# Optimization experiments

Measured on AMD Instinct MI355X. Metric: run time of the kernel, lower is better.

## Reference

```python
import jax, jax.numpy as jnp
import numpy as np

# Dimensions: batch B, window W (time features), nodes M, hidden HID, hops NLAYERS
B, W, M, HID, NLAYERS = 32, 168, 2048, 128, 6


def setup_inputs() -> dict:
    key = jax.random.key(0)
    ks = jax.random.split(key, 6)
    x = jax.random.normal(ks[0], (B, W, M), dtype=jnp.float32)
    # scale L so matrix powers L^k stay bounded (spectral radius < 1)
    L = jax.random.normal(ks[1], (M, M), dtype=jnp.float32) / (2.0 * np.float32(np.sqrt(M)))
    # stacked per-hop MLP params: linears[i]: W->HID, linears2[i]: HID->1
    W1 = jax.random.normal(ks[2], (NLAYERS + 1, HID, W), dtype=jnp.float32) / np.float32(np.sqrt(W))
    b1 = jax.random.normal(ks[3], (NLAYERS + 1, HID), dtype=jnp.float32) * 0.01
    W2 = jax.random.normal(ks[4], (NLAYERS + 1, HID), dtype=jnp.float32) / np.float32(np.sqrt(HID))
    b2 = jax.random.normal(ks[5], (NLAYERS + 1,), dtype=jnp.float32) * 0.01
    return {"x": x, "L": L, "W1": W1, "b1": b1, "W2": W2, "b2": b2}


def _hop_mlp(t, w1, bb1, w2, bb2):
    # t: [B, M, W] -> scalar score per node: Linear(W->HID), ReLU, Linear(HID->1)
    h = jax.nn.relu(jnp.einsum('bmw,hw->bmh', t, w1) + bb1)
    return jnp.einsum('bmh,h->bm', h, w2) + bb2


def reference(x, L, W1, b1, W2, b2):
    xt = jnp.swapaxes(x, 1, 2)  # [B, M, W] (x.transpose(2,1))
    s = _hop_mlp(xt, W1[0], b1[0], W2[0], b2[0])  # [B, M]
    P = L
    for i in range(1, NLAYERS + 1):
        # PP.expand + bmm == broadcasted matmul; never materialize [B,M,M]
        t = jnp.einsum('ij,bjw->biw', P, xt)  # [B, M, W]
        s = s + _hop_mlp(t, W1[i], b1[i], W2[i], b2[i])
        P = jnp.matmul(L, P)  # next graph power
    return s  # [B, M]; output_fun is None so no final nonlinearity
```

## Files before the change

### kernel.cpp

```cpp
#include <hip/hip_runtime.h>
#include <cstdint>
#include <cstddef>

typedef __bf16 bf16_t;
typedef __attribute__((ext_vector_type(8))) __bf16 bf16x8;
typedef __attribute__((ext_vector_type(4))) __bf16 bf16x4;
typedef __attribute__((ext_vector_type(4))) float floatx4;

#define NB 32
#define NW 168
#define NM 2048
#define NHID 128
#define NBW (NB * NW)
#define NGEMM 168
#define NMLPB 512

#define GLOAD_LDS16(g, l)                                          \
  __builtin_amdgcn_global_load_lds(                                \
      (const __attribute__((address_space(1))) void*)(g),          \
      (__attribute__((address_space(3))) void*)(l), 16, 0, 0)

__global__ void cast_bf16_kernel(const float* __restrict__ in, bf16_t* __restrict__ out, int n4) {
  int stride = gridDim.x * blockDim.x;
  for (int i = blockIdx.x * blockDim.x + threadIdx.x; i < n4; i += stride) {
    float4 v = ((const float4*)in)[i];
    bf16x4 o = {(bf16_t)v.x, (bf16_t)v.y, (bf16_t)v.z, (bf16_t)v.w};
    ((bf16x4*)out)[i] = o;
  }
}

__global__ void prep_x_kernel(const float* __restrict__ x, bf16_t* __restrict__ Xb,
                              bf16_t* __restrict__ XT) {
  __shared__ float tile[64][65];
  const int R = NBW, C = NM;
  int r0 = blockIdx.y * 64, c0 = blockIdx.x * 64;
  int t = threadIdx.x;
  int tr = t >> 4, tc4 = (t & 15) * 4;
#pragma unroll
  for (int p = 0; p < 4; ++p) {
    int row = p * 16 + tr;
    float4 v = *(const float4*)(x + (size_t)(r0 + row) * C + c0 + tc4);
    tile[row][tc4 + 0] = v.x;
    tile[row][tc4 + 1] = v.y;
    tile[row][tc4 + 2] = v.z;
    tile[row][tc4 + 3] = v.w;
    bf16x4 o = {(bf16_t)v.x, (bf16_t)v.y, (bf16_t)v.z, (bf16_t)v.w};
    *(bf16x4*)(Xb + (size_t)(r0 + row) * C + c0 + tc4) = o;
  }
  __syncthreads();
#pragma unroll
  for (int p = 0; p < 4; ++p) {
    int c = p * 16 + tr;
    bf16x4 o = {(bf16_t)tile[tc4 + 0][c], (bf16_t)tile[tc4 + 1][c],
                (bf16_t)tile[tc4 + 2][c], (bf16_t)tile[tc4 + 3][c]};
    *(bf16x4*)(XT + (size_t)(c0 + c) * R + r0 + tc4) = o;
  }
}

__device__ __forceinline__ void mlp_single(
    int tid, int r0, bf16_t* __restrict__ Bs,
    const bf16_t* __restrict__ T, const bf16_t* __restrict__ Wh,
    const float* __restrict__ b1h, const float* __restrict__ w2h, float b2v,
    float* __restrict__ out, int accumulate) {
  float* sred = (float*)(Bs + 24576);
  int lane = tid & 63, wv2 = tid >> 6;

#pragma unroll
  for (int i = 0; i < 6; ++i) {
    int c = i * 512 + tid;
    if (c >= 2688) {
      int4 z = {0, 0, 0, 0};
      *(int4*)(Bs + (size_t)c * 8) = z;
    } else {
      int kc = c >> 7;
      int h = (c & 127) ^ ((kc & 3) << 2);
      GLOAD_LDS16(Wh + (size_t)h * NW + kc * 8, Bs + (size_t)(i * 512 + wv2 * 64) * 8);
    }
  }
  __syncthreads();

  if (tid < 256) {
    int wm = wv2 >> 1, wn = wv2 & 1;
    int quad = lane >> 4, l15 = lane & 15;
    const bf16_t* arow[4];
#pragma unroll
    for (int mi = 0; mi < 4; ++mi) {
      int R = r0 + wm * 64 + mi * 16 + l15;
      arow[mi] = T + (size_t)(R >> 5) * NBW + (size_t)(R & 31) * NW + quad * 8;
    }
    floatx4 zero4 = {0.f, 0.f, 0.f, 0.f};
    floatx4 acc[4][4];
#pragma unroll
    for (int mi = 0; mi < 4; ++mi)
#pragma unroll
      for (int ni = 0; ni < 4; ++ni) acc[mi][ni] = zero4;

#pragma unroll
    for (int kb = 0; kb < 192; kb += 32) {
      int kc = (kb >> 3) + quad;
      bf16x8 af[4], bf[4];
#pragma unroll
      for (int mi = 0; mi < 4; ++mi)
        af[mi] = *(const bf16x8*)(arow[mi] + kb);
#pragma unroll
      for (int ni = 0; ni < 4; ++ni) {
        int hpos = (wn * 64 + ni * 16 + l15) ^ ((kc & 3) << 2);
        bf[ni] = *(const bf16x8*)(Bs + (size_t)(kc * 128 + hpos) * 8);
      }
#pragma unroll
      for (int mi = 0; mi < 4; ++mi)
#pragma unroll
        for (int ni = 0; ni < 4; ++ni)
          acc[mi][ni] = __builtin_amdgcn_mfma_f32_16x16x32_bf16(af[mi], bf[ni], acc[mi][ni], 0, 0, 0);
    }

    float part[4][4];
#pragma unroll
    for (int mi = 0; mi < 4; ++mi)
#pragma unroll
      for (int r = 0; r < 4; ++r) part[mi][r] = 0.f;
#pragma unroll
    for (int ni = 0; ni < 4; ++ni) {
      int col = wn * 64 + ni * 16 + l15;
      float b1v = b1h[col];
      float w2v = w2h[col];
#pragma unroll
      for (int mi = 0; mi < 4; ++mi)
#pragma unroll
        for (int r = 0; r < 4; ++r) {
          float h = acc[mi][ni][r] + b1v;
          h = h > 0.f ? h : 0.f;
          part[mi][r] += h * w2v;
        }
    }
#pragma unroll
    for (int off = 1; off < 16; off <<= 1)
#pragma unroll
      for (int mi = 0; mi < 4; ++mi)
#pragma unroll
        for (int r = 0; r < 4; ++r) part[mi][r] += __shfl_xor(part[mi][r], off);
    if (l15 == 0) {
#pragma unroll
      for (int mi = 0; mi < 4; ++mi)
#pragma unroll
        for (int r = 0; r < 4; ++r) sred[wv2 * 64 + mi * 16 + quad * 4 + r] = part[mi][r];
    }
  }
  __syncthreads();
  if (tid < 128) {
    int hh = tid >> 6;
    int lr = tid & 63;
    float v = sred[(hh * 2) * 64 + lr] + sred[(hh * 2 + 1) * 64 + lr] + b2v;
    int R = r0 + hh * 64 + lr;
    int idx = (R & 31) * NM + (R >> 5);
    if (accumulate)
      out[idx] += v;
    else
      out[idx] = v;
  }
}

#define STAGE2(gbase, ld, t, ks, ldsbase)                                        \
  do {                                                                           \
    const bf16_t* _g = (gbase) + (size_t)(t) * 64 + (ks) * 32;                   \
    GLOAD_LDS16(_g, lds + (ldsbase) + (ks) * 8192 + wv * 512);                   \
    GLOAD_LDS16(_g + (size_t)128 * (ld),                                         \
                lds + (ldsbase) + (ks) * 8192 + 4096 + wv * 512);                \
  } while (0)

#define VM6 asm volatile("s_waitcnt vmcnt(6)" ::: "memory")
#define TOPB asm volatile("s_barrier" ::: "memory")
#define ENDB __builtin_amdgcn_s_barrier()

#define RD_A(dst, bufoff, ks, mh)                                                \
  _Pragma("unroll") for (int mi = 0; mi < 4; ++mi)                               \
      dst[mi] = *(const bf16x8*)(pA + (bufoff) + (ks) * 8192 + ((mh) * 4 + mi) * 512)

#define RD_B(dst, bufoff, ks)                                                    \
  _Pragma("unroll") for (int ni = 0; ni < 4; ++ni)                               \
      dst[ni] = *(const bf16x8*)(pB + (bufoff) + (ks) * 8192 + ni * 512)

#define MM16(af_, bf_, mh)                                                       \
  do {                                                                           \
    __builtin_amdgcn_s_setprio(1);                                               \
    _Pragma("unroll") for (int mi = 0; mi < 4; ++mi)                             \
        _Pragma("unroll") for (int ni = 0; ni < 4; ++ni)                         \
            acc[(mh) * 4 + mi][ni] = __builtin_amdgcn_mfma_f32_16x16x32_bf16(    \
                af_[mi], bf_[ni], acc[(mh) * 4 + mi][ni], 0, 0, 0);              \
    __builtin_amdgcn_s_setprio(0);                                               \
  } while (0)

__global__ __launch_bounds__(512, 2) void fused_gemm_mlp_kernel(
    const bf16_t* __restrict__ A, const bf16_t* __restrict__ Bt,
    bf16_t* __restrict__ C, bf16_t* __restrict__ Ct,
    int K, int lda, int ldb, int ldc, int ldct, int write_c,
    const bf16_t* __restrict__ T, const bf16_t* __restrict__ W1b,
    const float* __restrict__ b1, const float* __restrict__ W2,
    const float* __restrict__ b2, float* __restrict__ out,
    int hop, int accumulate) {
  __shared__ bf16_t lds[65536];
  const int bx = blockIdx.x;
  const int tid = threadIdx.x;

  if (bx >= NGEMM) {
    int j = bx - NGEMM;
    mlp_single(tid, j * 128, lds, T, W1b + (size_t)hop * NHID * NW,
               b1 + hop * NHID, W2 + hop * NHID, b2[hop], out, accumulate);
    return;
  }

  const int m0 = (bx >> 3) * 256, n0 = (bx & 7) * 256;
  const int lane = tid & 63, wv = tid >> 6;
  const int wm = wv >> 2, wn = wv & 3;
  const int quad = lane >> 4, l15 = lane & 15;

  const int srow = tid >> 2;
  const int scsw = (tid & 3) ^ ((srow >> 1) & 3);
  const bf16_t* aS = A + (size_t)(m0 + srow) * lda + scsw * 8;
  const bf16_t* bS = Bt + (size_t)(n0 + srow) * ldb + scsw * 8;

  const int fsw = (quad ^ ((l15 >> 1) & 3)) * 8;
  const bf16_t* pA = lds + (size_t)(wm * 128 + l15) * 32 + fsw;
  const bf16_t* pB = lds + 16384 + (size_t)(wn * 64 + l15) * 32 + fsw;

  floatx4 zero4 = {0.f, 0.f, 0.f, 0.f};
  floatx4 acc[8][4];
#pragma unroll
  for (int mi = 0; mi < 8; ++mi)
#pragma unroll
    for (int ni = 0; ni < 4; ++ni) acc[mi][ni] = zero4;

  STAGE2(aS, lda, 0, 0, 0);
  STAGE2(bS, ldb, 0, 0, 16384);
  STAGE2(aS, lda, 0, 1, 0);
  STAGE2(bS, ldb, 0, 1, 16384);
  STAGE2(aS, lda, 1, 0, 32768);
  STAGE2(bS, ldb, 1, 0, 49152);
  asm volatile("s_waitcnt vmcnt(8)" ::: "memory");
  TOPB;

  bf16x8 af0[4], af1[4], bf0[4], bf1[4];
  RD_B(bf0, 0, 0);
  RD_A(af0, 0, 0, 0);

  const int nt = K >> 6;
  const int nit = K >> 7;
#pragma unroll 1
  for (int i = 0; i < nit; ++i) {
    const int t1 = 2 * i + 1;
    const int t2 = (t1 + 1 < nt) ? t1 + 1 : 0;
    const int t3 = (t1 + 2 < nt) ? t1 + 2 : 0;
    RD_A(af1, 0, 0, 1);
    MM16(af0, bf0, 0);
    STAGE2(aS, lda, t1, 1, 32768);
    ENDB;
    VM6; TOPB;
    RD_B(bf1, 0, 1);
    RD_A(af0, 0, 1, 0);
    MM16(af1, bf0, 1);
    STAGE2(bS, ldb, t1, 1, 49152);
    ENDB;
    RD_A(af1, 0, 1, 1);
    MM16(af0, bf1, 0);
    STAGE2(aS, lda, t2, 0, 0);
    ENDB;
    VM6; TOPB;
    RD_B(bf0, 32768, 0);
    RD_A(af0, 32768, 0, 0);
    MM16(af1, bf1, 1);
    STAGE2(bS, ldb, t2, 0, 16384);
    ENDB;
    RD_A(af1, 32768, 0, 1);
    MM16(af0, bf0, 0);
    STAGE2(aS, lda, t2, 1, 0);
    ENDB;
    VM6; TOPB;
    RD_B(bf1, 32768, 1);
    RD_A(af0, 32768, 1, 0);
    MM16(af1, bf0, 1);
    STAGE2(bS, ldb, t2, 1, 16384);
    ENDB;
    RD_A(af1, 32768, 1, 1);
    MM16(af0, bf1, 0);
    STAGE2(aS, lda, t3, 0, 32768);
    ENDB;
    VM6; TOPB;
    RD_B(bf0, 0, 0);
    RD_A(af0, 0, 0, 0);
    MM16(af1, bf1, 1);
    STAGE2(bS, ldb, t3, 0, 49152);
    ENDB;
  }
  asm volatile("s_waitcnt vmcnt(0)" ::: "memory");

#pragma unroll
  for (int mi = 0; mi < 8; ++mi) {
#pragma unroll
    for (int ni = 0; ni < 4; ++ni) {
      int col = n0 + wn * 64 + ni * 16 + l15;
      int rowb = m0 + wm * 128 + mi * 16 + quad * 4;
      bf16x4 tv;
#pragma unroll
      for (int r = 0; r < 4; ++r) tv[r] = (bf16_t)acc[mi][ni][r];
      *(bf16x4*)(Ct + (size_t)col * ldct + rowb) = tv;
      if (write_c) {
#pragma unroll
        for (int r = 0; r < 4; ++r)
          C[(size_t)(rowb + r) * ldc + col] = tv[r];
      }
    }
  }
}

__global__ __launch_bounds__(512) void mlp_score_kernel(
    const bf16_t* __restrict__ T, const bf16_t* __restrict__ W1b,
    const float* __restrict__ b1, const float* __restrict__ W2,
    const float* __restrict__ b2, float* __restrict__ out,
    int hop, int accumulate) {
  __shared__ bf16_t Bs[24 * 128 * 8 + 512];
  mlp_single(threadIdx.x, blockIdx.x * 128, Bs, T,
             W1b + (size_t)hop * NHID * NW, b1 + hop * NHID, W2 + hop * NHID,
             b2[hop], out, accumulate);
}

extern "C" void kernel_launch(void* const* d_in, const int* in_sizes, int n_in,
                              void* d_out, int out_size, void* d_ws, size_t ws_size,
                              hipStream_t stream) {
  const float* x = (const float*)d_in[0];
  const float* L = (const float*)d_in[1];
  const float* W1 = (const float*)d_in[2];
  const float* b1 = (const float*)d_in[3];
  const float* W2 = (const float*)d_in[4];
  const float* b2 = (const float*)d_in[5];
  float* out = (float*)d_out;

  char* ws = (char*)d_ws;
  size_t off = 0;
  auto walloc = [&](size_t bytes) -> void* {
    off = (off + 255) & ~(size_t)255;
    void* p = ws + off;
    off += bytes;
    return p;
  };
  bf16_t* Xb = (bf16_t*)walloc((size_t)NBW * NM * 2);
  bf16_t* XT0 = (bf16_t*)walloc((size_t)NM * NBW * 2);
  bf16_t* XT1 = (bf16_t*)walloc((size_t)NM * NBW * 2);
  bf16_t* Lb = (bf16_t*)walloc((size_t)NM * NM * 2);
  bf16_t* W1b = (bf16_t*)walloc((size_t)7 * NHID * NW * 2);
  bf16_t* Ta = (bf16_t*)walloc((size_t)NBW * NM * 2);
  (void)ws_size; (void)in_sizes; (void)n_in; (void)out_size;

  prep_x_kernel<<<dim3(NM / 64, NBW / 64), dim3(256), 0, stream>>>(x, Xb, XT0);
  cast_bf16_kernel<<<dim3(1024), dim3(256), 0, stream>>>(L, Lb, NM * NM / 4);
  cast_bf16_kernel<<<dim3(64), dim3(256), 0, stream>>>(W1, W1b, 7 * NHID * NW / 4);

  bf16_t* src = Xb;
  bf16_t* dst = Ta;
  bf16_t* xtprev = XT0;
  bf16_t* xtcur = XT1;
  for (int i = 1; i <= 6; ++i) {
    fused_gemm_mlp_kernel<<<dim3(NGEMM + NMLPB), dim3(512), 0, stream>>>(
        src, Lb, dst, xtcur, NM, NM, NM, NM, NBW, (i < 6) ? 1 : 0,
        xtprev, W1b, b1, W2, b2, out, i - 1, (i > 1) ? 1 : 0);
    bf16_t* t = src; src = dst; dst = t;
    t = xtprev; xtprev = xtcur; xtcur = t;
  }
  mlp_score_kernel<<<dim3(NM * NB / 128), dim3(512), 0, stream>>>(
      xtprev, W1b, b1, W2, b2, out, 6, 1);
}
```

Before: 466.0 us.

## Use 32x32x16 MFMA in GEMM, widen MLP blocks, merge prep kernels

Switches the main GEMM inner loop from 16x16x32 to 32x32x16 bf16 MFMA tiles, changing LDS fragment reads, swizzle and epilogue layout to match. The MLP-score path now uses all 8 waves to process 256 rows per block, which halves the number of MLP blocks. The three prep kernels (x transpose/cast, L cast, W1 cast) are merged into one launch. The aim is fewer LDS reads per FLOP, better MFMA efficiency and less launch overhead. The risks are register pressure from the floatx16 accumulators and a possible layout mismatch in the new fragment indexing.

```diff
diff --git a/kernel.cpp b/kernel.cpp
--- a/kernel.cpp
+++ b/kernel.cpp
@@ -6,6 +6,7 @@
 typedef __attribute__((ext_vector_type(8))) __bf16 bf16x8;
 typedef __attribute__((ext_vector_type(4))) __bf16 bf16x4;
 typedef __attribute__((ext_vector_type(4))) float floatx4;
+typedef __attribute__((ext_vector_type(16))) float floatx16;
 
 #define NB 32
 #define NW 168
@@ -13,51 +14,61 @@
 #define NHID 128
 #define NBW (NB * NW)
 #define NGEMM 168
-#define NMLPB 512
+#define NMLPB 256
 
 #define GLOAD_LDS16(g, l)                                          \
   __builtin_amdgcn_global_load_lds(                                \
       (const __attribute__((address_space(1))) void*)(g),          \
       (__attribute__((address_space(3))) void*)(l), 16, 0, 0)
 
-__global__ void cast_bf16_kernel(const float* __restrict__ in, bf16_t* __restrict__ out, int n4) {
-  int stride = gridDim.x * blockDim.x;
-  for (int i = blockIdx.x * blockDim.x + threadIdx.x; i < n4; i += stride) {
-    float4 v = ((const float4*)in)[i];
-    bf16x4 o = {(bf16_t)v.x, (bf16_t)v.y, (bf16_t)v.z, (bf16_t)v.w};
-    ((bf16x4*)out)[i] = o;
-  }
-}
-
-__global__ void prep_x_kernel(const float* __restrict__ x, bf16_t* __restrict__ Xb,
-                              bf16_t* __restrict__ XT) {
+__global__ void prep_all_kernel(const float* __restrict__ x, bf16_t* __restrict__ Xb,
+                                bf16_t* __restrict__ XT, const float* __restrict__ L,
+                                bf16_t* __restrict__ Lb, const float* __restrict__ W1,
+                                bf16_t* __restrict__ W1b) {
   __shared__ float tile[64][65];
-  const int R = NBW, C = NM;
-  int r0 = blockIdx.y * 64, c0 = blockIdx.x * 64;
-  int t = threadIdx.x;
-  int tr = t >> 4, tc4 = (t & 15) * 4;
-#pragma unroll
-  for (int p = 0; p < 4; ++p) {
-    int row = p * 16 + tr;
-    float4 v = *(const float4*)(x + (size_t)(r0 + row) * C + c0 + tc4);
-    tile[row][tc4 + 0] = v.x;
-    tile[row][tc4 + 1] = v.y;
-    tile[row][tc4 + 2] = v.z;
-    tile[row][tc4 + 3] = v.w;
-    bf16x4 o = {(bf16_t)v.x, (bf16_t)v.y, (bf16_t)v.z, (bf16_t)v.w};
-    *(bf16x4*)(Xb + (size_t)(r0 + row) * C + c0 + tc4) = o;
-  }
-  __syncthreads();
-#pragma unroll
-  for (int p = 0; p < 4; ++p) {
-    int c = p * 16 + tr;
-    bf16x4 o = {(bf16_t)tile[tc4 + 0][c], (bf16_t)tile[tc4 + 1][c],
-                (bf16_t)tile[tc4 + 2][c], (bf16_t)tile[tc4 + 3][c]};
-    *(bf16x4*)(XT + (size_t)(c0 + c) * R + r0 + tc4) = o;
-  }
-}
-
-__device__ __forceinline__ void mlp_single(
+  const int bx = blockIdx.x;
+  const int t = threadIdx.x;
+  if (bx < 2688) {
+    const int R = NBW, C = NM;
+    int r0 = (bx >> 5) * 64, c0 = (bx & 31) * 64;
+    int tr = t >> 4, tc4 = (t & 15) * 4;
+#pragma unroll
+    for (int p = 0; p < 4; ++p) {
+      int row = p * 16 + tr;
+      float4 v = *(const float4*)(x + (size_t)(r0 + row) * C + c0 + tc4);
+      tile[row][tc4 + 0] = v.x;
+      tile[row][tc4 + 1] = v.y;
+      tile[row][tc4 + 2] = v.z;
+      tile[row][tc4 + 3] = v.w;
+      bf16x4 o = {(bf16_t)v.x, (bf16_t)v.y, (bf16_t)v.z, (bf16_t)v.w};
+      *(bf16x4*)(Xb + (size_t)(r0 + row) * C + c0 + tc4) = o;
+    }
+    __syncthreads();
+#pragma unroll
+    for (int p = 0; p < 4; ++p) {
+      int c = p * 16 + tr;
+      bf16x4 o = {(bf16_t)tile[tc4 + 0][c], (bf16_t)tile[tc4 + 1][c],
+                  (bf16_t)tile[tc4 + 2][c], (bf16_t)tile[tc4 + 3][c]};
+      *(bf16x4*)(XT + (size_t)(c0 + c) * R + r0 + tc4) = o;
+    }
+  } else if (bx < 3712) {
+    const int n4 = NM * NM / 4;
+    for (int i = (bx - 2688) * 256 + t; i < n4; i += 1024 * 256) {
+      float4 v = ((const float4*)L)[i];
+      bf16x4 o = {(bf16_t)v.x, (bf16_t)v.y, (bf16_t)v.z, (bf16_t)v.w};
+      ((bf16x4*)Lb)[i] = o;
+    }
+  } else {
+    const int n4 = 7 * NHID * NW / 4;
+    for (int i = (bx - 3712) * 256 + t; i < n4; i += 64 * 256) {
+      float4 v = ((const float4*)W1)[i];
+      bf16x4 o = {(bf16_t)v.x, (bf16_t)v.y, (bf16_t)v.z, (bf16_t)v.w};
+      ((bf16x4*)W1b)[i] = o;
+    }
+  }
+}
+
+__device__ __forceinline__ void mlp_block(
     int tid, int r0, bf16_t* __restrict__ Bs,
     const bf16_t* __restrict__ T, const bf16_t* __restrict__ Wh,
     const float* __restrict__ b1h, const float* __restrict__ w2h, float b2v,
@@ -79,7 +90,7 @@
   }
   __syncthreads();
 
-  if (tid < 256) {
+  {
     int wm = wv2 >> 1, wn = wv2 & 1;
     int quad = lane >> 4, l15 = lane & 15;
     const bf16_t* arow[4];
@@ -147,11 +158,11 @@
     }
   }
   __syncthreads();
-  if (tid < 128) {
-    int hh = tid >> 6;
+  if (tid < 256) {
+    int wm = tid >> 6;
     int lr = tid & 63;
-    float v = sred[(hh * 2) * 64 + lr] + sred[(hh * 2 + 1) * 64 + lr] + b2v;
-    int R = r0 + hh * 64 + lr;
+    float v = sred[(wm * 2) * 64 + lr] + sred[(wm * 2 + 1) * 64 + lr] + b2v;
+    int R = r0 + wm * 64 + lr;
     int idx = (R & 31) * NM + (R >> 5);
     if (accumulate)
       out[idx] += v;
@@ -172,21 +183,27 @@
 #define TOPB asm volatile("s_barrier" ::: "memory")
 #define ENDB __builtin_amdgcn_s_barrier()
 
-#define RD_A(dst, bufoff, ks, mh)                                                \
-  _Pragma("unroll") for (int mi = 0; mi < 4; ++mi)                               \
-      dst[mi] = *(const bf16x8*)(pA + (bufoff) + (ks) * 8192 + ((mh) * 4 + mi) * 512)
-
-#define RD_B(dst, bufoff, ks)                                                    \
-  _Pragma("unroll") for (int ni = 0; ni < 4; ++ni)                               \
-      dst[ni] = *(const bf16x8*)(pB + (bufoff) + (ks) * 8192 + ni * 512)
-
-#define MM16(af_, bf_, mh)                                                       \
+#define RD_A4(dst, bufoff, ks, mh)                                               \
+  _Pragma("unroll") for (int kk = 0; kk < 2; ++kk)                               \
+      _Pragma("unroll") for (int mf = 0; mf < 2; ++mf)                           \
+          dst[kk * 2 + mf] = *(const bf16x8*)(pA + (bufoff) + (ks) * 8192 +      \
+              ((mh) * 2 + mf) * 1024 + (((kk * 2 + hi) ^ fsw32) << 3))
+
+#define RD_B4(dst, bufoff, ks)                                                   \
+  _Pragma("unroll") for (int kk = 0; kk < 2; ++kk)                               \
+      _Pragma("unroll") for (int nf = 0; nf < 2; ++nf)                           \
+          dst[kk * 2 + nf] = *(const bf16x8*)(pB + (bufoff) + (ks) * 8192 +      \
+              nf * 1024 + (((kk * 2 + hi) ^ fsw32) << 3))
+
+#define MM(af_, bf_, mh)                                                         \
   do {                                                                           \
     __builtin_amdgcn_s_setprio(1);                                               \
-    _Pragma("unroll") for (int mi = 0; mi < 4; ++mi)                             \
-        _Pragma("unroll") for (int ni = 0; ni < 4; ++ni)                         \
-            acc[(mh) * 4 + mi][ni] = __builtin_amdgcn_mfma_f32_16x16x32_bf16(    \
-                af_[mi], bf_[ni], acc[(mh) * 4 + mi][ni], 0, 0, 0);              \
+    _Pragma("unroll") for (int mf = 0; mf < 2; ++mf)                             \
+        _Pragma("unroll") for (int nf = 0; nf < 2; ++nf)                         \
+            _Pragma("unroll") for (int kk = 0; kk < 2; ++kk)                     \
+                acc[(mh) * 2 + mf][nf] = __builtin_amdgcn_mfma_f32_32x32x16_bf16(\
+                    af_[kk * 2 + mf], bf_[kk * 2 + nf], acc[(mh) * 2 + mf][nf],  \
+                    0, 0, 0);                                                    \
     __builtin_amdgcn_s_setprio(0);                                               \
   } while (0)
 
@@ -204,31 +221,32 @@
 
   if (bx >= NGEMM) {
     int j = bx - NGEMM;
-    mlp_single(tid, j * 128, lds, T, W1b + (size_t)hop * NHID * NW,
-               b1 + hop * NHID, W2 + hop * NHID, b2[hop], out, accumulate);
+    mlp_block(tid, j * 256, lds, T, W1b + (size_t)hop * NHID * NW,
+              b1 + hop * NHID, W2 + hop * NHID, b2[hop], out, accumulate);
     return;
   }
 
   const int m0 = (bx >> 3) * 256, n0 = (bx & 7) * 256;
   const int lane = tid & 63, wv = tid >> 6;
   const int wm = wv >> 2, wn = wv & 3;
-  const int quad = lane >> 4, l15 = lane & 15;
+  const int l31 = lane & 31, hi = lane >> 5;
+  const int fsw32 = (l31 >> 1) & 3;
 
   const int srow = tid >> 2;
   const int scsw = (tid & 3) ^ ((srow >> 1) & 3);
   const bf16_t* aS = A + (size_t)(m0 + srow) * lda + scsw * 8;
   const bf16_t* bS = Bt + (size_t)(n0 + srow) * ldb + scsw * 8;
 
-  const int fsw = (quad ^ ((l15 >> 1) & 3)) * 8;
-  const bf16_t* pA = lds + (size_t)(wm * 128 + l15) * 32 + fsw;
-  const bf16_t* pB = lds + 16384 + (size_t)(wn * 64 + l15) * 32 + fsw;
-
-  floatx4 zero4 = {0.f, 0.f, 0.f, 0.f};
-  floatx4 acc[8][4];
-#pragma unroll
-  for (int mi = 0; mi < 8; ++mi)
-#pragma unroll
-    for (int ni = 0; ni < 4; ++ni) acc[mi][ni] = zero4;
+  const bf16_t* pA = lds + (size_t)(wm * 128 + l31) * 32;
+  const bf16_t* pB = lds + 16384 + (size_t)(wn * 64 + l31) * 32;
+
+  floatx16 acc[4][2];
+#pragma unroll
+  for (int mf = 0; mf < 4; ++mf)
+#pragma unroll
+    for (int nf = 0; nf < 2; ++nf)
+#pragma unroll
+      for (int r = 0; r < 16; ++r) acc[mf][nf][r] = 0.f;
 
   STAGE2(aS, lda, 0, 0, 0);
   STAGE2(bS, ldb, 0, 0, 16384);
@@ -240,8 +258,8 @@
   TOPB;
 
   bf16x8 af0[4], af1[4], bf0[4], bf1[4];
-  RD_B(bf0, 0, 0);
-  RD_A(af0, 0, 0, 0);
+  RD_B4(bf0, 0, 0);
+  RD_A4(af0, 0, 0, 0);
 
   const int nt = K >> 6;
   const int nit = K >> 7;
@@ -250,63 +268,66 @@
     const int t1 = 2 * i + 1;
     const int t2 = (t1 + 1 < nt) ? t1 + 1 : 0;
     const int t3 = (t1 + 2 < nt) ? t1 + 2 : 0;
-    RD_A(af1, 0, 0, 1);
-    MM16(af0, bf0, 0);
+    RD_A4(af1, 0, 0, 1);
+    MM(af0, bf0, 0);
     STAGE2(aS, lda, t1, 1, 32768);
     ENDB;
     VM6; TOPB;
-    RD_B(bf1, 0, 1);
-    RD_A(af0, 0, 1, 0);
-    MM16(af1, bf0, 1);
+    RD_B4(bf1, 0, 1);
+    RD_A4(af0, 0, 1, 0);
+    MM(af1, bf0, 1);
     STAGE2(bS, ldb, t1, 1, 49152);
     ENDB;
-    RD_A(af1, 0, 1, 1);
-    MM16(af0, bf1, 0);
+    RD_A4(af1, 0, 1, 1);
+    MM(af0, bf1, 0);
     STAGE2(aS, lda, t2, 0, 0);
     ENDB;
     VM6; TOPB;
-    RD_B(bf0, 32768, 0);
-    RD_A(af0, 32768, 0, 0);
-    MM16(af1, bf1, 1);
+    RD_B4(bf0, 32768, 0);
+    RD_A4(af0, 32768, 0, 0);
+    MM(af1, bf1, 1);
     STAGE2(bS, ldb, t2, 0, 16384);
     ENDB;
-    RD_A(af1, 32768, 0, 1);
-    MM16(af0, bf0, 0);
+    RD_A4(af1, 32768, 0, 1);
+    MM(af0, bf0, 0);
     STAGE2(aS, lda, t2, 1, 0);
     ENDB;
     VM6; TOPB;
-    RD_B(bf1, 32768, 1);
-    RD_A(af0, 32768, 1, 0);
-    MM16(af1, bf0, 1);
+    RD_B4(bf1, 32768, 1);
+    RD_A4(af0, 32768, 1, 0);
+    MM(af1, bf0, 1);
     STAGE2(bS, ldb, t2, 1, 16384);
     ENDB;
-    RD_A(af1, 32768, 1, 1);
-    MM16(af0, bf1, 0);
+    RD_A4(af1, 32768, 1, 1);
+    MM(af0, bf1, 0);
     STAGE2(aS, lda, t3, 0, 32768);
     ENDB;
     VM6; TOPB;
-    RD_B(bf0, 0, 0);
-    RD_A(af0, 0, 0, 0);
-    MM16(af1, bf1, 1);
+    RD_B4(bf0, 0, 0);
+    RD_A4(af0, 0, 0, 0);
+    MM(af1, bf1, 1);
     STAGE2(bS, ldb, t3, 0, 49152);
     ENDB;
   }
   asm volatile("s_waitcnt vmcnt(0)" ::: "memory");
 
 #pragma unroll
-  for (int mi = 0; mi < 8; ++mi) {
-#pragma unroll
-    for (int ni = 0; ni < 4; ++ni) {
-      int col = n0 + wn * 64 + ni * 16 + l15;
-      int rowb = m0 + wm * 128 + mi * 16 + quad * 4;
-      bf16x4 tv;
-#pragma unroll
-      for (int r = 0; r < 4; ++r) tv[r] = (bf16_t)acc[mi][ni][r];
-      *(bf16x4*)(Ct + (size_t)col * ldct + rowb) = tv;
-      if (write_c) {
-#pragma unroll
-        for (int r = 0; r < 4; ++r)
-          C[(size_t)(rowb + r) * ldc + col] = tv[r];
+  for (int mf = 0; mf < 4; ++mf) {
+#pragma unroll
+    for (int nf = 0; nf < 2; ++nf) {
+      int col = n0 + wn * 64 + nf * 32 + l31;
+#pragma unroll
+      for (int g = 0; g < 4; ++g) {
+        int rowb = m0 + wm * 128 + mf * 32 + 4 * hi + 8 * g;
+        bf16x4 tv;
+#pragma unroll
+        for (int r = 0; r < 4; ++r) tv[r] = (bf16_t)acc[mf][nf][g * 4 + r];
+        *(bf16x4*)(Ct + (size_t)col * ldct + rowb) = tv;
+        if (write_c) {
+#pragma unroll
+          for (int r = 0; r < 4; ++r)
+            C[(size_t)(rowb + r) * ldc + col] = tv[r];
+        }
       }
     }
   }
@@ -317,10 +338,10 @@
     const float* __restrict__ b1, const float* __restrict__ W2,
     const float* __restrict__ b2, float* __restrict__ out,
     int hop, int accumulate) {
-  __shared__ bf16_t Bs[24 * 128 * 8 + 512];
-  mlp_single(threadIdx.x, blockIdx.x * 128, Bs, T,
-             W1b + (size_t)hop * NHID * NW, b1 + hop * NHID, W2 + hop * NHID,
-             b2[hop], out, accumulate);
+  __shared__ bf16_t Bs[25600];
+  mlp_block(threadIdx.x, blockIdx.x * 256, Bs, T,
+            W1b + (size_t)hop * NHID * NW, b1 + hop * NHID, W2 + hop * NHID,
+            b2[hop], out, accumulate);
 }
 
 extern "C" void kernel_launch(void* const* d_in, const int* in_sizes, int n_in,
@@ -350,9 +371,7 @@
   bf16_t* Ta = (bf16_t*)walloc((size_t)NBW * NM * 2);
   (void)ws_size; (void)in_sizes; (void)n_in; (void)out_size;
 
-  prep_x_kernel<<<dim3(NM / 64, NBW / 64), dim3(256), 0, stream>>>(x, Xb, XT0);
-  cast_bf16_kernel<<<dim3(1024), dim3(256), 0, stream>>>(L, Lb, NM * NM / 4);
-  cast_bf16_kernel<<<dim3(64), dim3(256), 0, stream>>>(W1, W1b, 7 * NHID * NW / 4);
+  prep_all_kernel<<<dim3(3776), dim3(256), 0, stream>>>(x, Xb, XT0, L, Lb, W1, W1b);
 
   bf16_t* src = Xb;
   bf16_t* dst = Ta;
@@ -365,6 +384,6 @@
     bf16_t* t = src; src = dst; dst = t;
     t = xtprev; xtprev = xtcur; xtcur = t;
   }
-  mlp_score_kernel<<<dim3(NM * NB / 128), dim3(512), 0, stream>>>(
+  mlp_score_kernel<<<dim3(NM * NB / 256), dim3(512), 0, stream>>>(
       xtprev, W1b, b1, W2, b2, out, 6, 1);
 }
```

After: 485.5 us. 4.2% more time.
